# Kernel optimization log

Measured on AMD Instinct MI355X. Metric: run time of the kernel, lower is better.

Reference implementation:

```python
import jax, jax.numpy as jnp
import numpy as np

STEP_PRI = 0.01
STEP_DUAL = 0.01
REG_SP = 0.002
NUM_ITERS = 50
B, N = 512, 64


def _matrix_power(m, p):
    # exponentiation by squaring; p is a static Python int >= 1
    result = jnp.broadcast_to(jnp.eye(m.shape[-1], dtype=m.dtype), m.shape)
    while p > 0:
        if p & 1:
            result = result @ m
        p >>= 1
        if p:
            m = m @ m
    return result


def _matrix_poly(m, d, p):
    # (I + m/d)^p, matching torch matrix_poly
    x = jnp.eye(d, dtype=m.dtype) + m / d
    return _matrix_power(x, p)


def _threshold(x):
    # nn.Threshold(0.5, 0): x if x > 0.5 else 0
    return jnp.where(x > 0.5, x, jnp.zeros_like(x))


def setup_inputs() -> dict:
    key = jax.random.key(0)
    adj = jax.random.uniform(key, (B, N, N), dtype=jnp.float32)
    return {"adj": adj}


def reference(adj):
    n = adj.shape[-1]
    x0 = adj
    scores = _threshold(adj)
    alpha0 = jnp.zeros(adj.shape[0], dtype=adj.dtype)

    def step(carry, _):
        x, alpha = carry
        # grad of augmented Lagrangian (DAG constraint gradient uses (I + x*x/n)^(n-1)^T)
        poly_t = jnp.swapaxes(_matrix_poly(x * x, n, n - 1), -1, -2)
        grad = -scores + 2.0 * alpha[:, None, None] * x * poly_t / n
        til_x = x - STEP_PRI * grad
        # soft-threshold (prox of L1), then clamp to <= 1
        new_x = jax.nn.relu(jnp.abs(til_x) - REG_SP * STEP_PRI)
        x = 1.0 - jax.nn.relu(1.0 - new_x)
        # constraint2: tr((I + x*x/n)^min(30,n)) / n - 1, per batch element
        h = jnp.trace(_matrix_poly(x * x, n, min(30, n)), axis1=-2, axis2=-1) / n - 1.0
        alpha = alpha + STEP_DUAL * h
        return (x, alpha), None

    (x, _), _ = jax.lax.scan(step, (x0, alpha0), None, length=NUM_ITERS)
    return _threshold(x)
```

## Files before the change

kernel.cpp:

```cpp
#include <hip/hip_runtime.h>
#include <stdint.h>

#define PL 4096

typedef unsigned int u32;
typedef unsigned short u16;
typedef float f32x4 __attribute__((ext_vector_type(4)));
typedef short short8 __attribute__((ext_vector_type(8)));

__device__ __forceinline__ u32 prm(u32 a, u32 b, u32 s) {
  return __builtin_amdgcn_perm(a, b, s);
}
__device__ __forceinline__ u32 pk(float f0, float f1) {
  return prm(__float_as_uint(f1), __float_as_uint(f0), 0x07060302u);
}
__device__ __forceinline__ float rlo(u32 w) { return __uint_as_float(w << 16); }
__device__ __forceinline__ float rhi(u32 w) {
  return __uint_as_float(w & 0xffff0000u);
}
__device__ __forceinline__ short8 mk8(u32 w0, u32 w1, u32 w2, u32 w3) {
  union {
    u32 w[4];
    short8 s;
  } u;
  u.w[0] = w0;
  u.w[1] = w1;
  u.w[2] = w2;
  u.w[3] = w3;
  return u.s;
}
__device__ __forceinline__ void dot8(short8 a, short8 b, float& part) {
  union {
    short8 s;
    u32 w[4];
  } ua, ub;
  ua.s = a;
  ub.s = b;
#pragma unroll
  for (int w = 0; w < 4; ++w) {
    part = fmaf(rlo(ua.w[w]), rlo(ub.w[w]), part);
    part = fmaf(rhi(ua.w[w]), rhi(ub.w[w]), part);
  }
}
__device__ __forceinline__ f32x4 MF(short8 a, short8 b, f32x4 c) {
  return __builtin_amdgcn_mfma_f32_16x16x32_bf16(a, b, c, 0, 0, 0);
}

struct AF {
  short8 a0, a1;
};
struct BF8 {
  short8 b[4][2];
};

__device__ __forceinline__ AF macc_to_af(const f32x4 (&m)[4]) {
  u32 P0[4], P1[4];
#pragma unroll
  for (int b = 0; b < 4; ++b) {
    P0[b] = pk(m[b][0], m[b][1]);
    P1[b] = pk(m[b][2], m[b][3]);
  }
  AF r;
  r.a0 = mk8(P0[0], P1[0], P0[1], P1[1]);
  r.a1 = mk8(P0[2], P1[2], P0[3], P1[3]);
  return r;
}

__global__ __launch_bounds__(256, 2) void dag_iter_kernel(
    const float* __restrict__ adj, float* __restrict__ out) {
  __shared__ __align__(16) u16 BUF[3 * PL];
  __shared__ float red[4];
  u16* SM = BUF;
  u16* P1 = BUF + PL;
  u16* P2 = BUF + 2 * PL;

  if ((blockIdx.x >> 8) & 1) __builtin_amdgcn_s_sleep(11);

  const int tid = (int)threadIdx.x;
  const int lane = tid & 63;
  const int wv = tid >> 6;
  const int l15 = lane & 15;
  const int grp = lane >> 4;
  const int l7 = l15 & 7;

  const int c = 16 * wv + l15;
  int rb[4][2];
#pragma unroll
  for (int b = 0; b < 4; ++b)
#pragma unroll
    for (int kh = 0; kh < 2; ++kh)
      rb[b][kh] = (16 * b + l15) * 64 + ((((kh << 2) + grp) ^ l7) << 3);
  int sT[4];
#pragma unroll
  for (int b = 0; b < 4; ++b)
    sT[b] = (16 * b + l15) * 64 +
            ((((grp + ((wv >> 1) << 2)) ^ ((16 * b + l15) & 7))) << 3) +
            ((wv & 1) << 2);
  int stT[2];
#pragma unroll
  for (int h = 0; h < 2; ++h)
    stT[h] = c * 64 + ((((h << 2) + grp) ^ (c & 7)) << 3);

  AF afI;
  {
    const bool mine = (grp == (l15 >> 2));
    const int s = ((wv & 1) << 2) + (l15 & 3);
    const u32 onev = (s & 1) ? 0x3F800000u : 0x00003F80u;
    u32 w[4];
#pragma unroll
    for (int k = 0; k < 4; ++k) w[k] = (mine && ((s >> 1) == k)) ? onev : 0u;
    short8 hot = mk8(w[0], w[1], w[2], w[3]);
    short8 zero = mk8(0u, 0u, 0u, 0u);
    afI.a0 = (wv < 2) ? hot : zero;
    afI.a1 = (wv < 2) ? zero : hot;
  }

  const float* src = adj + (size_t)blockIdx.x * 4096;
  float x[4][4], sc[4][4];
#pragma unroll
  for (int b = 0; b < 4; ++b)
#pragma unroll
    for (int j = 0; j < 4; ++j) {
      float v = src[(16 * b + 4 * grp + j) * 64 + c];
      x[b][j] = v;
      sc[b][j] = (v > 0.5f) ? v : 0.0f;
    }
  float alpha = 0.0f;
  AF af;
  BF8 bf3;
  f32x4 acc63[4];

  auto loadBF = [&](const u16* P) {
    BF8 f;
#pragma unroll
    for (int b = 0; b < 4; ++b) {
      f.b[b][0] = *(const short8*)(P + rb[b][0]);
      f.b[b][1] = *(const short8*)(P + rb[b][1]);
    }
    return f;
  };
  auto mirrorAF = [&](const AF& a, const BF8& bf) {
    const f32x4 Z = {0.0f, 0.0f, 0.0f, 0.0f};
    f32x4 m[4];
    __builtin_amdgcn_s_setprio(1);
#pragma unroll
    for (int b = 0; b < 4; ++b) {
      m[b] = MF(bf.b[b][0], a.a0, Z);
      m[b] = MF(bf.b[b][1], a.a1, m[b]);
    }
    __builtin_amdgcn_s_setprio(0);
    return macc_to_af(m);
  };
  auto primaryT = [&](const AF& a, const BF8& bf, u16* P) {
    const f32x4 Z = {0.0f, 0.0f, 0.0f, 0.0f};
    f32x4 p[4];
    __builtin_amdgcn_s_setprio(1);
#pragma unroll
    for (int b = 0; b < 4; ++b) {
      p[b] = MF(a.a0, bf.b[b][0], Z);
      p[b] = MF(a.a1, bf.b[b][1], p[b]);
    }
    __builtin_amdgcn_s_setprio(0);
#pragma unroll
    for (int b = 0; b < 4; ++b)
      *(uint2*)(P + sT[b]) =
          make_uint2(pk(p[b][0], p[b][1]), pk(p[b][2], p[b][3]));
  };
  auto traceP = [&](const AF& a, const BF8& bf) {
    short8 c0s = bf.b[0][0], c1s = bf.b[0][1];
    if (wv == 1) {
      c0s = bf.b[1][0];
      c1s = bf.b[1][1];
    } else if (wv == 2) {
      c0s = bf.b[2][0];
      c1s = bf.b[2][1];
    } else if (wv == 3) {
      c0s = bf.b[3][0];
      c1s = bf.b[3][1];
    }
    float part = 0.0f;
    dot8(a.a0, c0s, part);
    dot8(a.a1, c1s, part);
#pragma unroll
    for (int off = 1; off < 64; off <<= 1) part += __shfl_xor(part, off);
    if (lane == 0) red[wv] = part;
  };

  auto prox = [&](float til[4][4]) {
#pragma unroll
    for (int b = 0; b < 4; ++b)
#pragma unroll
      for (int j = 0; j < 4; ++j) {
        float ax = fabsf(til[b][j]) - 2e-5f;
        x[b][j] = fminf(fmaxf(ax, 0.0f), 1.0f);
      }
  };
  auto stage = [&]() {
    float m[4][4];
#pragma unroll
    for (int b = 0; b < 4; ++b)
#pragma unroll
      for (int j = 0; j < 4; ++j)
        m[b][j] = fmaf(x[b][j] * x[b][j], 0.015625f,
                       (b == wv && 4 * grp + j == l15) ? 1.0f : 0.0f);
#pragma unroll
    for (int h = 0; h < 2; ++h)
      *(short8*)(SM + stT[h]) =
          mk8(pk(m[2 * h][0], m[2 * h][1]), pk(m[2 * h][2], m[2 * h][3]),
              pk(m[2 * h + 1][0], m[2 * h + 1][1]),
              pk(m[2 * h + 1][2], m[2 * h + 1][3]));
    __syncthreads();
  };
  auto gradprox = [&]() {
    float tr = red[0] + red[1] + red[2] + red[3];
    alpha = fmaf(0.01f, tr * 0.015625f - 1.0f, alpha);
    const float a2 = alpha * 0.03125f;
    float til[4][4];
#pragma unroll
    for (int b = 0; b < 4; ++b)
#pragma unroll
      for (int j = 0; j < 4; ++j) {
        float g = fmaf(a2 * x[b][j], acc63[b][j], -sc[b][j]);
        til[b][j] = fmaf(-0.01f, g, x[b][j]);
      }
    prox(til);
  };

  auto chain = [&]() {
    BF8 bm = loadBF(SM);
    AF afm = mirrorAF(afI, bm);
    AF af2 = mirrorAF(afm, bm);
    AF af3 = mirrorAF(af2, bm);
    primaryT(af2, bm, P1);
    __syncthreads();
    bf3 = loadBF(P1);
    AF af6 = mirrorAF(af3, bf3);
    AF af9 = mirrorAF(af6, bf3);
    AF af12 = mirrorAF(af9, bf3);
    af = mirrorAF(af12, bf3);
    primaryT(af12, bf3, P2);
    __syncthreads();
  };
  auto front = [&]() {
    BF8 b15 = loadBF(P2);
    traceP(af, b15);
    __syncthreads();
    AF af30 = mirrorAF(af, b15);
    AF af45 = mirrorAF(af30, b15);
    AF af60 = mirrorAF(af45, b15);
    const f32x4 Z = {0.0f, 0.0f, 0.0f, 0.0f};
    __builtin_amdgcn_s_setprio(1);
#pragma unroll
    for (int b = 0; b < 4; ++b) {
      acc63[b] = MF(bf3.b[b][0], af60.a0, Z);
      acc63[b] = MF(bf3.b[b][1], af60.a1, acc63[b]);
    }
    __builtin_amdgcn_s_setprio(0);
  };

  {
    float til[4][4];
#pragma unroll
    for (int b = 0; b < 4; ++b)
#pragma unroll
      for (int j = 0; j < 4; ++j) til[b][j] = fmaf(0.01f, sc[b][j], x[b][j]);
    prox(til);
    stage();
    chain();
  }
  for (int it = 0; it < 48; ++it) {
    front();
    gradprox();
    stage();
    chain();
  }
  front();
  gradprox();

  float* dst = out + (size_t)blockIdx.x * 4096;
#pragma unroll
  for (int b = 0; b < 4; ++b)
#pragma unroll
    for (int j = 0; j < 4; ++j) {
      float v = x[b][j];
      dst[(16 * b + 4 * grp + j) * 64 + c] = (v > 0.5f) ? v : 0.0f;
    }
}

extern "C" void kernel_launch(void* const* d_in, const int* in_sizes, int n_in,
                              void* d_out, int out_size, void* d_ws,
                              size_t ws_size, hipStream_t stream) {
  const float* adj = (const float*)d_in[0];
  float* out = (float*)d_out;
  const int nbatch = in_sizes[0] / 4096;
  dag_iter_kernel<<<nbatch, 256, 0, stream>>>(adj, out);
}
```

Measured before the change: 183.5 us.

## Pack two matrices per block with phase-offset barriers to overlap their chains

Each block now processes two batch matrices with 512 threads, each half having its own LDS region. The second half enters two extra barriers at the start and the first half two extra barriers at the end, so the halves run staggered by two barrier phases. The intent is to interleave one matrix's MFMA chain with the other's sync and elementwise phases, replacing the earlier s_sleep-based staggering between separate blocks. This relies on both halves reaching exactly matching barrier counts and doubles the LDS used per block.

```diff
diff --git a/kernel.cpp b/kernel.cpp
--- a/kernel.cpp
+++ b/kernel.cpp
@@ -66,24 +66,25 @@
   return r;
 }
 
-__global__ __launch_bounds__(256, 2) void dag_iter_kernel(
+__global__ __launch_bounds__(512, 2) void dag_iter_kernel(
     const float* __restrict__ adj, float* __restrict__ out) {
-  __shared__ __align__(16) u16 BUF[3 * PL];
-  __shared__ float red[4];
-  u16* SM = BUF;
-  u16* P1 = BUF + PL;
-  u16* P2 = BUF + 2 * PL;
-
-  if ((blockIdx.x >> 8) & 1) __builtin_amdgcn_s_sleep(11);
+  __shared__ __align__(16) u16 BUF[6 * PL];
+  __shared__ float red[8];
 
   const int tid = (int)threadIdx.x;
   const int lane = tid & 63;
   const int wv = tid >> 6;
+  const int mat = wv >> 2;
+  const int w = wv & 3;
   const int l15 = lane & 15;
   const int grp = lane >> 4;
   const int l7 = l15 & 7;
 
-  const int c = 16 * wv + l15;
+  u16* SM = BUF + mat * 3 * PL;
+  u16* P1 = SM + PL;
+  u16* P2 = SM + 2 * PL;
+
+  const int c = 16 * w + l15;
   int rb[4][2];
 #pragma unroll
   for (int b = 0; b < 4; ++b)
@@ -94,8 +95,8 @@
 #pragma unroll
   for (int b = 0; b < 4; ++b)
     sT[b] = (16 * b + l15) * 64 +
-            ((((grp + ((wv >> 1) << 2)) ^ ((16 * b + l15) & 7))) << 3) +
-            ((wv & 1) << 2);
+            ((((grp + ((w >> 1) << 2)) ^ ((16 * b + l15) & 7))) << 3) +
+            ((w & 1) << 2);
   int stT[2];
 #pragma unroll
   for (int h = 0; h < 2; ++h)
@@ -104,18 +105,18 @@
   AF afI;
   {
     const bool mine = (grp == (l15 >> 2));
-    const int s = ((wv & 1) << 2) + (l15 & 3);
+    const int s = ((w & 1) << 2) + (l15 & 3);
     const u32 onev = (s & 1) ? 0x3F800000u : 0x00003F80u;
-    u32 w[4];
-#pragma unroll
-    for (int k = 0; k < 4; ++k) w[k] = (mine && ((s >> 1) == k)) ? onev : 0u;
-    short8 hot = mk8(w[0], w[1], w[2], w[3]);
+    u32 ww[4];
+#pragma unroll
+    for (int k = 0; k < 4; ++k) ww[k] = (mine && ((s >> 1) == k)) ? onev : 0u;
+    short8 hot = mk8(ww[0], ww[1], ww[2], ww[3]);
     short8 zero = mk8(0u, 0u, 0u, 0u);
-    afI.a0 = (wv < 2) ? hot : zero;
-    afI.a1 = (wv < 2) ? zero : hot;
-  }
-
-  const float* src = adj + (size_t)blockIdx.x * 4096;
+    afI.a0 = (w < 2) ? hot : zero;
+    afI.a1 = (w < 2) ? zero : hot;
+  }
+
+  const float* src = adj + (size_t)(2 * blockIdx.x + mat) * 4096;
   float x[4][4], sc[4][4];
 #pragma unroll
   for (int b = 0; b < 4; ++b)
@@ -127,6 +128,7 @@
     }
   float alpha = 0.0f;
   AF af;
+  AF af3;
   BF8 bf3;
   f32x4 acc63[4];
 
@@ -168,13 +170,13 @@
   };
   auto traceP = [&](const AF& a, const BF8& bf) {
     short8 c0s = bf.b[0][0], c1s = bf.b[0][1];
-    if (wv == 1) {
+    if (w == 1) {
       c0s = bf.b[1][0];
       c1s = bf.b[1][1];
-    } else if (wv == 2) {
+    } else if (w == 2) {
       c0s = bf.b[2][0];
       c1s = bf.b[2][1];
-    } else if (wv == 3) {
+    } else if (w == 3) {
       c0s = bf.b[3][0];
       c1s = bf.b[3][1];
     }
@@ -183,7 +185,7 @@
     dot8(a.a1, c1s, part);
 #pragma unroll
     for (int off = 1; off < 64; off <<= 1) part += __shfl_xor(part, off);
-    if (lane == 0) red[wv] = part;
+    if (lane == 0) red[(mat << 2) + w] = part;
   };
 
   auto prox = [&](float til[4][4]) {
@@ -195,14 +197,14 @@
         x[b][j] = fminf(fmaxf(ax, 0.0f), 1.0f);
       }
   };
-  auto stage = [&]() {
+  auto stageW = [&]() {
     float m[4][4];
 #pragma unroll
     for (int b = 0; b < 4; ++b)
 #pragma unroll
       for (int j = 0; j < 4; ++j)
         m[b][j] = fmaf(x[b][j] * x[b][j], 0.015625f,
-                       (b == wv && 4 * grp + j == l15) ? 1.0f : 0.0f);
+                       (b == w && 4 * grp + j == l15) ? 1.0f : 0.0f);
 #pragma unroll
     for (int h = 0; h < 2; ++h)
       *(short8*)(SM + stT[h]) =
@@ -212,7 +214,8 @@
     __syncthreads();
   };
   auto gradprox = [&]() {
-    float tr = red[0] + red[1] + red[2] + red[3];
+    const int rbase = mat << 2;
+    float tr = red[rbase] + red[rbase + 1] + red[rbase + 2] + red[rbase + 3];
     alpha = fmaf(0.01f, tr * 0.015625f - 1.0f, alpha);
     const float a2 = alpha * 0.03125f;
     float til[4][4];
@@ -226,13 +229,15 @@
     prox(til);
   };
 
-  auto chain = [&]() {
+  auto segHEAD = [&]() {
     BF8 bm = loadBF(SM);
     AF afm = mirrorAF(afI, bm);
     AF af2 = mirrorAF(afm, bm);
-    AF af3 = mirrorAF(af2, bm);
+    af3 = mirrorAF(af2, bm);
     primaryT(af2, bm, P1);
     __syncthreads();
+  };
+  auto segTAIL = [&]() {
     bf3 = loadBF(P1);
     AF af6 = mirrorAF(af3, bf3);
     AF af9 = mirrorAF(af6, bf3);
@@ -241,10 +246,9 @@
     primaryT(af12, bf3, P2);
     __syncthreads();
   };
-  auto front = [&]() {
+  auto segFRONT = [&]() {
     BF8 b15 = loadBF(P2);
     traceP(af, b15);
-    __syncthreads();
     AF af30 = mirrorAF(af, b15);
     AF af45 = mirrorAF(af30, b15);
     AF af60 = mirrorAF(af45, b15);
@@ -256,7 +260,13 @@
       acc63[b] = MF(bf3.b[b][1], af60.a1, acc63[b]);
     }
     __builtin_amdgcn_s_setprio(0);
-  };
+    __syncthreads();
+  };
+
+  if (mat) {
+    __builtin_amdgcn_s_barrier();
+    __builtin_amdgcn_s_barrier();
+  }
 
   {
     float til[4][4];
@@ -265,19 +275,21 @@
 #pragma unroll
       for (int j = 0; j < 4; ++j) til[b][j] = fmaf(0.01f, sc[b][j], x[b][j]);
     prox(til);
-    stage();
-    chain();
-  }
+    stageW();
+  }
+  segHEAD();
+  segTAIL();
   for (int it = 0; it < 48; ++it) {
-    front();
+    segFRONT();
     gradprox();
-    stage();
-    chain();
-  }
-  front();
+    stageW();
+    segHEAD();
+    segTAIL();
+  }
+  segFRONT();
   gradprox();
 
-  float* dst = out + (size_t)blockIdx.x * 4096;
+  float* dst = out + (size_t)(2 * blockIdx.x + mat) * 4096;
 #pragma unroll
   for (int b = 0; b < 4; ++b)
 #pragma unroll
@@ -285,6 +297,11 @@
       float v = x[b][j];
       dst[(16 * b + 4 * grp + j) * 64 + c] = (v > 0.5f) ? v : 0.0f;
     }
+
+  if (mat == 0) {
+    __builtin_amdgcn_s_barrier();
+    __builtin_amdgcn_s_barrier();
+  }
 }
 
 extern "C" void kernel_launch(void* const* d_in, const int* in_sizes, int n_in,
@@ -293,5 +310,5 @@
   const float* adj = (const float*)d_in[0];
   float* out = (float*)d_out;
   const int nbatch = in_sizes[0] / 4096;
-  dag_iter_kernel<<<nbatch, 256, 0, stream>>>(adj, out);
-}
+  dag_iter_kernel<<<nbatch / 2, 512, 0, stream>>>(adj, out);
+}
```

Result: slower. 198.6 us (+8.2%).
